# Kernel tuning notes

Measured on AMD Instinct MI355X. Metric: run time of the kernel, lower is better.

The kernel has to match this reference:

```python
import jax, jax.numpy as jnp
import numpy as np

F_IN, N_TREES, DEPTH, TREE_DIM, BATCH = 256, 512, 6, 3, 512


def entmax15_axis0(z):
    """Exact 1.5-entmax along axis 0 (sort-based algorithm from Peters et al. 2019)."""
    z = z / 2.0
    z = z - jnp.max(z, axis=0, keepdims=True)
    zs = -jnp.sort(-z, axis=0)                      # descending sort, [F, N]
    F = z.shape[0]
    rho = jnp.arange(1, F + 1, dtype=z.dtype)[:, None]
    mean = jnp.cumsum(zs, axis=0) / rho
    mean_sq = jnp.cumsum(zs * zs, axis=0) / rho
    ss = rho * (mean_sq - mean * mean)
    delta = (1.0 - ss) / rho
    tau = mean - jnp.sqrt(jnp.clip(delta, 0.0))
    support = (tau <= zs).astype(jnp.int32)
    k = jnp.sum(support, axis=0) - 1                # last valid index per column
    tau_star = jnp.take_along_axis(tau, k[None, :], axis=0)
    return jnp.square(jnp.clip(z - tau_star, 0.0))


def setup_inputs() -> dict:
    key = jax.random.key(0)
    k0, k1, k2, k3 = jax.random.split(key, 4)
    return {
        "input": jax.random.normal(k0, (BATCH, F_IN), jnp.float32),
        "feat_attention": jax.random.uniform(k1, (F_IN, N_TREES * DEPTH), jnp.float32),
        "feature_thresholds": jax.random.normal(k2, (N_TREES, DEPTH), jnp.float32) * 0.1,
        "log_temperatures": jnp.zeros((N_TREES, DEPTH), jnp.float32),
        "response": jax.random.normal(k3, (N_TREES, TREE_DIM, 2 ** DEPTH), jnp.float32),
    }


def reference(input, feat_attention, feature_thresholds, log_temperatures, response):
    T, D = feature_thresholds.shape
    F = feat_attention.shape[0]
    # sparse feature selection per (tree, depth)
    choice_weight = entmax15_axis0(feat_attention).reshape(F, T, D)
    feature_values = jnp.einsum('bi,ind->bnd', input, choice_weight)      # [B, T, D]
    # thresholding with learned temperature, bin_func == '05_01'
    tl = (feature_values - feature_thresholds) * jnp.exp(-log_temperatures)
    tl = jnp.stack([-tl, tl], axis=-1)                                    # [B, T, D, 2]
    bins = jnp.clip(0.5 * tl + 0.5, -0.5, 1.5)
    # binary codes of the 2^D leaves: [D, 2^D, 2]
    idx = jnp.arange(2 ** D)
    off = 2 ** jnp.arange(D)
    bc = ((idx[None, :] // off[:, None]) % 2).astype(bins.dtype)
    codes = jnp.stack([bc, 1.0 - bc], axis=-1)
    # depth-wise outer product into leaf weights
    bin_matches = jnp.einsum('btds,dcs->btdc', bins, codes)               # [B, T, D, 2^D]
    response_weights = jnp.prod(bin_matches, axis=-2)                     # [B, T, 2^D]
    out = jnp.einsum('bnd,ncd->bnc', response_weights, response)          # [B, T, C]
    return out.reshape(out.shape[0], -1)
```

## Files before the change

kernel.cpp:

```cpp
#include <hip/hip_runtime.h>
#include <math.h>

#define F_IN 256
#define NTREES 512
#define DEPTH 6
#define NCOLS (NTREES * DEPTH)
#define BATCH 512
#define OUTW (NTREES * 3)

typedef __attribute__((ext_vector_type(8))) short bf16x8;
typedef __attribute__((ext_vector_type(4))) float f32x4;
typedef __attribute__((ext_vector_type(8))) unsigned short u16x8;

__device__ __forceinline__ unsigned short f2bf(float x) {
    unsigned u = __float_as_uint(x);
    return (unsigned short)((u + 0x7FFFu + ((u >> 16) & 1u)) >> 16);
}
__device__ __forceinline__ void split2(float x, unsigned short& h, unsigned short& l) {
    h = f2bf(x);
    l = f2bf(x - __uint_as_float((unsigned)h << 16));
}

__global__ __launch_bounds__(256) void k_entmax(const float* __restrict__ att,
                                                unsigned short* __restrict__ cwT_hi,
                                                unsigned short* __restrict__ cwT_lo) {
    const int tid = threadIdx.x;
    const int n0 = blockIdx.x * 16;
    const int lane = tid & 63;
    const int w = tid >> 6;
    const int g = lane >> 4;
    const int li = lane & 15;

    __shared__ __align__(16) float s_z[16][260];

    const int cld = tid & 15;
#pragma unroll
    for (int it = 0; it < 16; ++it) {
        int f = (tid >> 4) + it * 16;
        s_z[cld][f] = att[f * NCOLS + n0 + cld];
    }
    __syncthreads();

    const int c = w * 4 + g;
    float4 z[4];
#pragma unroll
    for (int j = 0; j < 4; ++j) {
        float4 v = *(const float4*)&s_z[c][li * 16 + 4 * j];
        z[j] = make_float4(v.x * 0.5f, v.y * 0.5f, v.z * 0.5f, v.w * 0.5f);
    }
    float m = fmaxf(fmaxf(fmaxf(z[0].x, z[0].y), fmaxf(z[0].z, z[0].w)),
                    fmaxf(fmaxf(z[1].x, z[1].y), fmaxf(z[1].z, z[1].w)));
    m = fmaxf(m, fmaxf(fmaxf(fmaxf(z[2].x, z[2].y), fmaxf(z[2].z, z[2].w)),
                       fmaxf(fmaxf(z[3].x, z[3].y), fmaxf(z[3].z, z[3].w))));
#pragma unroll
    for (int off = 8; off >= 1; off >>= 1) m = fmaxf(m, __shfl_xor(m, off));
#pragma unroll
    for (int j = 0; j < 4; ++j) {
        z[j].x -= m; z[j].y -= m; z[j].z -= m; z[j].w -= m;
    }

    float tau = -1.0f;
    for (int iter = 0; iter < 14; ++iter) {
        float s1p[4], s2p[4];
#pragma unroll
        for (int j = 0; j < 4; ++j) {
            float d0 = fmaxf(z[j].x - tau, 0.f);
            float d1 = fmaxf(z[j].y - tau, 0.f);
            float d2 = fmaxf(z[j].z - tau, 0.f);
            float d3 = fmaxf(z[j].w - tau, 0.f);
            s1p[j] = (d0 + d1) + (d2 + d3);
            s2p[j] = fmaf(d0, d0, fmaf(d1, d1, fmaf(d2, d2, d3 * d3)));
        }
        float s1 = (s1p[0] + s1p[1]) + (s1p[2] + s1p[3]);
        float s2 = (s2p[0] + s2p[1]) + (s2p[2] + s2p[3]);
#pragma unroll
        for (int off = 8; off >= 1; off >>= 1) {
            s1 += __shfl_xor(s1, off);
            s2 += __shfl_xor(s2, off);
        }
        tau += (s2 - 1.f) / (2.f * s1);
        if (__all(fabsf(s2 - 1.f) < 4e-6f)) break;
    }

#pragma unroll
    for (int j = 0; j < 4; ++j) {
        float4 pv;
        float v0 = fmaxf(z[j].x - tau, 0.f);
        float v1 = fmaxf(z[j].y - tau, 0.f);
        float v2 = fmaxf(z[j].z - tau, 0.f);
        float v3 = fmaxf(z[j].w - tau, 0.f);
        pv.x = v0 * v0; pv.y = v1 * v1; pv.z = v2 * v2; pv.w = v3 * v3;
        *(float4*)&s_z[c][li * 16 + 4 * j] = pv;
    }
    __syncthreads();

    const int nl = tid >> 4;
    const int f0 = (tid & 15) * 16;
#pragma unroll
    for (int jj = 0; jj < 2; ++jj) {
        u16x8 hv, lv;
#pragma unroll
        for (int e = 0; e < 8; ++e) {
            unsigned short h, l;
            split2(s_z[nl][f0 + jj * 8 + e], h, l);
            hv[e] = h; lv[e] = l;
        }
        *(u16x8*)&cwT_hi[(n0 + nl) * F_IN + f0 + jj * 8] = hv;
        *(u16x8*)&cwT_lo[(n0 + nl) * F_IN + f0 + jj * 8] = lv;
    }
}

__global__ __launch_bounds__(512) void k_fused(const unsigned short* __restrict__ Ah,
                                               const unsigned short* __restrict__ Al,
                                               const float* __restrict__ inp,
                                               const float* __restrict__ thr,
                                               const float* __restrict__ ltemp,
                                               const float* __restrict__ resp,
                                               float* __restrict__ out) {
    const int tb  = blockIdx.x;
    const int b0  = blockIdx.y * 128;
    const int t0g = tb * 8;
    const int n0g = tb * 48;
    const int tid = threadIdx.x;
    const int wave = tid >> 6, lane = tid & 63;
    const int quad = lane >> 4, lr = lane & 15;

    __shared__ float sFV[48][132];
    __shared__ float sO[128][25];

    const int bw = b0 + wave * 16;
    const unsigned short* pah = Ah + (n0g + lr) * F_IN + quad * 8;
    const unsigned short* pal = Al + (n0g + lr) * F_IN + quad * 8;
    const float* pbf = inp + (bw + lr) * F_IN + quad * 8;

    f32x4 acc[3];
#pragma unroll
    for (int i = 0; i < 3; ++i) acc[i] = (f32x4){0.f, 0.f, 0.f, 0.f};

#pragma unroll
    for (int k0 = 0; k0 < F_IN; k0 += 32) {
        bf16x8 ah[3], al[3], bh, bl;
#pragma unroll
        for (int i = 0; i < 3; ++i) {
            ah[i] = *(const bf16x8*)(pah + i * 16 * F_IN + k0);
            al[i] = *(const bf16x8*)(pal + i * 16 * F_IN + k0);
        }
        float4 v0 = *(const float4*)(pbf + k0);
        float4 v1 = *(const float4*)(pbf + k0 + 4);
        float fb[8] = {v0.x, v0.y, v0.z, v0.w, v1.x, v1.y, v1.z, v1.w};
#pragma unroll
        for (int e = 0; e < 8; ++e) {
            unsigned short hh, ll;
            split2(fb[e], hh, ll);
            bh[e] = (short)hh; bl[e] = (short)ll;
        }
#pragma unroll
        for (int i = 0; i < 3; ++i) {
            acc[i] = __builtin_amdgcn_mfma_f32_16x16x32_bf16(ah[i], bh, acc[i], 0, 0, 0);
            acc[i] = __builtin_amdgcn_mfma_f32_16x16x32_bf16(ah[i], bl, acc[i], 0, 0, 0);
            acc[i] = __builtin_amdgcn_mfma_f32_16x16x32_bf16(al[i], bh, acc[i], 0, 0, 0);
        }
    }
#pragma unroll
    for (int i = 0; i < 3; ++i)
#pragma unroll
        for (int r = 0; r < 4; ++r)
            sFV[16 * i + quad * 4 + r][wave * 16 + lr] = acc[i][r];
    __syncthreads();

#pragma unroll
    for (int p = 0; p < 2; ++p) {
        const int pi = p * 512 + tid;
        const int tl = pi >> 7;
        const int b  = pi & 127;
        const int tls = __builtin_amdgcn_readfirstlane(tl);
        const float* rp = resp + (size_t)(t0g + tls) * 192;
        const float* tp = thr   + (t0g + tls) * 6;
        const float* lp = ltemp + (t0g + tls) * 6;

        float bpos[6], bneg[6];
#pragma unroll
        for (int d = 0; d < 6; ++d) {
            float fvv = sFV[tls * 6 + d][b];
            float tlv = (fvv - tp[d]) * __expf(-lp[d]);
            float hp = 0.5f * tlv + 0.5f;
            float hn = 0.5f - 0.5f * tlv;
            bpos[d] = fminf(fmaxf(hp, -0.5f), 1.5f);
            bneg[d] = fminf(fmaxf(hn, -0.5f), 1.5f);
        }
        float pr[64];
        pr[0] = 1.f;
#pragma unroll
        for (int d = 0; d < 6; ++d) {
            int half = 1 << d;
#pragma unroll 32
            for (int i = half - 1; i >= 0; --i) {
                float v = pr[i];
                pr[i + half] = v * bneg[d];
                pr[i]        = v * bpos[d];
            }
        }
        float a0 = 0.f, a1 = 0.f, a2 = 0.f;
#pragma unroll
        for (int cc = 0; cc < 64; ++cc) {
            a0 = fmaf(pr[cc], rp[cc], a0);
            a1 = fmaf(pr[cc], rp[64 + cc], a1);
            a2 = fmaf(pr[cc], rp[128 + cc], a2);
        }
        sO[b][tl * 3 + 0] = a0;
        sO[b][tl * 3 + 1] = a1;
        sO[b][tl * 3 + 2] = a2;
    }
    __syncthreads();
    for (int i = tid; i < 128 * 24; i += 512) {
        int row = i / 24, col = i % 24;
        out[(b0 + row) * OUTW + t0g * 3 + col] = sO[row][col];
    }
}

extern "C" void kernel_launch(void* const* d_in, const int* in_sizes, int n_in,
                              void* d_out, int out_size, void* d_ws, size_t ws_size,
                              hipStream_t stream) {
    const float* input = (const float*)d_in[0];
    const float* att   = (const float*)d_in[1];
    const float* thr   = (const float*)d_in[2];
    const float* ltemp = (const float*)d_in[3];
    const float* resp  = (const float*)d_in[4];
    float* out = (float*)d_out;

    unsigned short* cwT_hi = (unsigned short*)d_ws;
    unsigned short* cwT_lo = cwT_hi + NCOLS * F_IN;

    hipLaunchKernelGGL(k_entmax, dim3(NCOLS / 16), dim3(256), 0, stream,
                       att, cwT_hi, cwT_lo);
    hipLaunchKernelGGL(k_fused, dim3(NTREES / 8, BATCH / 128), dim3(512), 0, stream,
                       cwT_hi, cwT_lo, input, thr, ltemp, resp, out);
}
```

Baseline: 90.79 us.

## Fuse entmax into main kernel, computing weights in shared memory per block

Removes the separate entmax kernel and its global bf16 hi/lo workspace. Each block of the fused kernel now loads its 48 attention columns, runs the entmax bisection/Newton iteration in shared memory (8 threads per column), and splits to bf16 hi/lo on the fly when feeding MFMA. Shared memory is reused through a union for the later stages. This saves a launch and a global round trip, but entmax is recomputed redundantly by the 4 batch-tile blocks per tree group. Shared memory use per block also grows, which may lower occupancy.

```diff
diff --git a/kernel.cpp b/kernel.cpp
--- a/kernel.cpp
+++ b/kernel.cpp
@@ -10,7 +10,6 @@
 
 typedef __attribute__((ext_vector_type(8))) short bf16x8;
 typedef __attribute__((ext_vector_type(4))) float f32x4;
-typedef __attribute__((ext_vector_type(8))) unsigned short u16x8;
 
 __device__ __forceinline__ unsigned short f2bf(float x) {
     unsigned u = __float_as_uint(x);
@@ -21,102 +20,12 @@
     l = f2bf(x - __uint_as_float((unsigned)h << 16));
 }
 
-__global__ __launch_bounds__(256) void k_entmax(const float* __restrict__ att,
-                                                unsigned short* __restrict__ cwT_hi,
-                                                unsigned short* __restrict__ cwT_lo) {
-    const int tid = threadIdx.x;
-    const int n0 = blockIdx.x * 16;
-    const int lane = tid & 63;
-    const int w = tid >> 6;
-    const int g = lane >> 4;
-    const int li = lane & 15;
-
-    __shared__ __align__(16) float s_z[16][260];
-
-    const int cld = tid & 15;
-#pragma unroll
-    for (int it = 0; it < 16; ++it) {
-        int f = (tid >> 4) + it * 16;
-        s_z[cld][f] = att[f * NCOLS + n0 + cld];
-    }
-    __syncthreads();
-
-    const int c = w * 4 + g;
-    float4 z[4];
-#pragma unroll
-    for (int j = 0; j < 4; ++j) {
-        float4 v = *(const float4*)&s_z[c][li * 16 + 4 * j];
-        z[j] = make_float4(v.x * 0.5f, v.y * 0.5f, v.z * 0.5f, v.w * 0.5f);
-    }
-    float m = fmaxf(fmaxf(fmaxf(z[0].x, z[0].y), fmaxf(z[0].z, z[0].w)),
-                    fmaxf(fmaxf(z[1].x, z[1].y), fmaxf(z[1].z, z[1].w)));
-    m = fmaxf(m, fmaxf(fmaxf(fmaxf(z[2].x, z[2].y), fmaxf(z[2].z, z[2].w)),
-                       fmaxf(fmaxf(z[3].x, z[3].y), fmaxf(z[3].z, z[3].w))));
-#pragma unroll
-    for (int off = 8; off >= 1; off >>= 1) m = fmaxf(m, __shfl_xor(m, off));
-#pragma unroll
-    for (int j = 0; j < 4; ++j) {
-        z[j].x -= m; z[j].y -= m; z[j].z -= m; z[j].w -= m;
-    }
-
-    float tau = -1.0f;
-    for (int iter = 0; iter < 14; ++iter) {
-        float s1p[4], s2p[4];
-#pragma unroll
-        for (int j = 0; j < 4; ++j) {
-            float d0 = fmaxf(z[j].x - tau, 0.f);
-            float d1 = fmaxf(z[j].y - tau, 0.f);
-            float d2 = fmaxf(z[j].z - tau, 0.f);
-            float d3 = fmaxf(z[j].w - tau, 0.f);
-            s1p[j] = (d0 + d1) + (d2 + d3);
-            s2p[j] = fmaf(d0, d0, fmaf(d1, d1, fmaf(d2, d2, d3 * d3)));
-        }
-        float s1 = (s1p[0] + s1p[1]) + (s1p[2] + s1p[3]);
-        float s2 = (s2p[0] + s2p[1]) + (s2p[2] + s2p[3]);
-#pragma unroll
-        for (int off = 8; off >= 1; off >>= 1) {
-            s1 += __shfl_xor(s1, off);
-            s2 += __shfl_xor(s2, off);
-        }
-        tau += (s2 - 1.f) / (2.f * s1);
-        if (__all(fabsf(s2 - 1.f) < 4e-6f)) break;
-    }
-
-#pragma unroll
-    for (int j = 0; j < 4; ++j) {
-        float4 pv;
-        float v0 = fmaxf(z[j].x - tau, 0.f);
-        float v1 = fmaxf(z[j].y - tau, 0.f);
-        float v2 = fmaxf(z[j].z - tau, 0.f);
-        float v3 = fmaxf(z[j].w - tau, 0.f);
-        pv.x = v0 * v0; pv.y = v1 * v1; pv.z = v2 * v2; pv.w = v3 * v3;
-        *(float4*)&s_z[c][li * 16 + 4 * j] = pv;
-    }
-    __syncthreads();
-
-    const int nl = tid >> 4;
-    const int f0 = (tid & 15) * 16;
-#pragma unroll
-    for (int jj = 0; jj < 2; ++jj) {
-        u16x8 hv, lv;
-#pragma unroll
-        for (int e = 0; e < 8; ++e) {
-            unsigned short h, l;
-            split2(s_z[nl][f0 + jj * 8 + e], h, l);
-            hv[e] = h; lv[e] = l;
-        }
-        *(u16x8*)&cwT_hi[(n0 + nl) * F_IN + f0 + jj * 8] = hv;
-        *(u16x8*)&cwT_lo[(n0 + nl) * F_IN + f0 + jj * 8] = lv;
-    }
-}
-
-__global__ __launch_bounds__(512) void k_fused(const unsigned short* __restrict__ Ah,
-                                               const unsigned short* __restrict__ Al,
-                                               const float* __restrict__ inp,
-                                               const float* __restrict__ thr,
-                                               const float* __restrict__ ltemp,
-                                               const float* __restrict__ resp,
-                                               float* __restrict__ out) {
+__global__ __launch_bounds__(512) void k_all(const float* __restrict__ att,
+                                             const float* __restrict__ inp,
+                                             const float* __restrict__ thr,
+                                             const float* __restrict__ ltemp,
+                                             const float* __restrict__ resp,
+                                             float* __restrict__ out) {
     const int tb  = blockIdx.x;
     const int b0  = blockIdx.y * 128;
     const int t0g = tb * 8;
@@ -125,12 +34,82 @@
     const int wave = tid >> 6, lane = tid & 63;
     const int quad = lane >> 4, lr = lane & 15;
 
-    __shared__ float sFV[48][132];
-    __shared__ float sO[128][25];
+    __shared__ union {
+        float z[48][260];
+        struct { float fv[48][132]; float o[128][25]; } p2;
+    } s;
+
+    {
+        const int c4 = tid & 15;
+        const int fr = tid >> 4;
+        if (c4 < 12) {
+#pragma unroll
+            for (int it = 0; it < 8; ++it) {
+                int f = fr + it * 32;
+                float4 v = *(const float4*)&att[f * NCOLS + n0g + 4 * c4];
+                s.z[4 * c4 + 0][f] = v.x;
+                s.z[4 * c4 + 1][f] = v.y;
+                s.z[4 * c4 + 2][f] = v.z;
+                s.z[4 * c4 + 3][f] = v.w;
+            }
+        }
+    }
+    __syncthreads();
+
+    if (wave < 6) {
+        const int c  = tid >> 3;
+        const int li = tid & 7;
+        float4 z[8];
+#pragma unroll
+        for (int j = 0; j < 8; ++j) {
+            float4 v = *(const float4*)&s.z[c][li * 32 + 4 * j];
+            z[j] = make_float4(v.x * 0.5f, v.y * 0.5f, v.z * 0.5f, v.w * 0.5f);
+        }
+        float m = -1e30f;
+#pragma unroll
+        for (int j = 0; j < 8; ++j)
+            m = fmaxf(m, fmaxf(fmaxf(z[j].x, z[j].y), fmaxf(z[j].z, z[j].w)));
+#pragma unroll
+        for (int off = 4; off >= 1; off >>= 1) m = fmaxf(m, __shfl_xor(m, off));
+#pragma unroll
+        for (int j = 0; j < 8; ++j) {
+            z[j].x -= m; z[j].y -= m; z[j].z -= m; z[j].w -= m;
+        }
+
+        float tau = -1.0f;
+        for (int iter = 0; iter < 14; ++iter) {
+            float s1 = 0.f, s2 = 0.f;
+#pragma unroll
+            for (int j = 0; j < 8; ++j) {
+                float d0 = fmaxf(z[j].x - tau, 0.f);
+                float d1 = fmaxf(z[j].y - tau, 0.f);
+                float d2 = fmaxf(z[j].z - tau, 0.f);
+                float d3 = fmaxf(z[j].w - tau, 0.f);
+                s1 += (d0 + d1) + (d2 + d3);
+                s2 = fmaf(d0, d0, fmaf(d1, d1, fmaf(d2, d2, fmaf(d3, d3, s2))));
+            }
+#pragma unroll
+            for (int off = 4; off >= 1; off >>= 1) {
+                s1 += __shfl_xor(s1, off);
+                s2 += __shfl_xor(s2, off);
+            }
+            tau += (s2 - 1.f) / (2.f * s1);
+            if (__all(fabsf(s2 - 1.f) < 4e-6f)) break;
+        }
+#pragma unroll
+        for (int j = 0; j < 8; ++j) {
+            float v0 = fmaxf(z[j].x - tau, 0.f);
+            float v1 = fmaxf(z[j].y - tau, 0.f);
+            float v2 = fmaxf(z[j].z - tau, 0.f);
+            float v3 = fmaxf(z[j].w - tau, 0.f);
+            float4 pv;
+            pv.x = v0 * v0; pv.y = v1 * v1; pv.z = v2 * v2; pv.w = v3 * v3;
+            *(float4*)&s.z[c][li * 32 + 4 * j] = pv;
+        }
+    }
+    __syncthreads();
 
     const int bw = b0 + wave * 16;
-    const unsigned short* pah = Ah + (n0g + lr) * F_IN + quad * 8;
-    const unsigned short* pal = Al + (n0g + lr) * F_IN + quad * 8;
     const float* pbf = inp + (bw + lr) * F_IN + quad * 8;
 
     f32x4 acc[3];
@@ -142,8 +121,15 @@
         bf16x8 ah[3], al[3], bh, bl;
 #pragma unroll
         for (int i = 0; i < 3; ++i) {
-            ah[i] = *(const bf16x8*)(pah + i * 16 * F_IN + k0);
-            al[i] = *(const bf16x8*)(pal + i * 16 * F_IN + k0);
+            float4 a0 = *(const float4*)&s.z[16 * i + lr][quad * 8 + k0];
+            float4 a1 = *(const float4*)&s.z[16 * i + lr][quad * 8 + k0 + 4];
+            float fa[8] = {a0.x, a0.y, a0.z, a0.w, a1.x, a1.y, a1.z, a1.w};
+#pragma unroll
+            for (int e = 0; e < 8; ++e) {
+                unsigned short hh, ll;
+                split2(fa[e], hh, ll);
+                ah[i][e] = (short)hh; al[i][e] = (short)ll;
+            }
         }
         float4 v0 = *(const float4*)(pbf + k0);
         float4 v1 = *(const float4*)(pbf + k0 + 4);
@@ -161,11 +147,13 @@
             acc[i] = __builtin_amdgcn_mfma_f32_16x16x32_bf16(al[i], bh, acc[i], 0, 0, 0);
         }
     }
+    __syncthreads();
+
 #pragma unroll
     for (int i = 0; i < 3; ++i)
 #pragma unroll
         for (int r = 0; r < 4; ++r)
-            sFV[16 * i + quad * 4 + r][wave * 16 + lr] = acc[i][r];
+            s.p2.fv[16 * i + quad * 4 + r][wave * 16 + lr] = acc[i][r];
     __syncthreads();
 
 #pragma unroll
@@ -174,14 +162,14 @@
         const int tl = pi >> 7;
         const int b  = pi & 127;
         const int tls = __builtin_amdgcn_readfirstlane(tl);
-        const float* rp = resp + (size_t)(t0g + tls) * 192;
+        const float* rp = resp  + (size_t)(t0g + tls) * 192;
         const float* tp = thr   + (t0g + tls) * 6;
         const float* lp = ltemp + (t0g + tls) * 6;
 
         float bpos[6], bneg[6];
 #pragma unroll
         for (int d = 0; d < 6; ++d) {
-            float fvv = sFV[tls * 6 + d][b];
+            float fvv = s.p2.fv[tls * 6 + d][b];
             float tlv = (fvv - tp[d]) * __expf(-lp[d]);
             float hp = 0.5f * tlv + 0.5f;
             float hn = 0.5f - 0.5f * tlv;
@@ -207,14 +195,14 @@
             a1 = fmaf(pr[cc], rp[64 + cc], a1);
             a2 = fmaf(pr[cc], rp[128 + cc], a2);
         }
-        sO[b][tl * 3 + 0] = a0;
-        sO[b][tl * 3 + 1] = a1;
-        sO[b][tl * 3 + 2] = a2;
+        s.p2.o[b][tl * 3 + 0] = a0;
+        s.p2.o[b][tl * 3 + 1] = a1;
+        s.p2.o[b][tl * 3 + 2] = a2;
     }
     __syncthreads();
     for (int i = tid; i < 128 * 24; i += 512) {
         int row = i / 24, col = i % 24;
-        out[(b0 + row) * OUTW + t0g * 3 + col] = sO[row][col];
+        out[(b0 + row) * OUTW + t0g * 3 + col] = s.p2.o[row][col];
     }
 }
 
@@ -227,12 +215,8 @@
     const float* ltemp = (const float*)d_in[3];
     const float* resp  = (const float*)d_in[4];
     float* out = (float*)d_out;
-
-    unsigned short* cwT_hi = (unsigned short*)d_ws;
-    unsigned short* cwT_lo = cwT_hi + NCOLS * F_IN;
-
-    hipLaunchKernelGGL(k_entmax, dim3(NCOLS / 16), dim3(256), 0, stream,
-                       att, cwT_hi, cwT_lo);
-    hipLaunchKernelGGL(k_fused, dim3(NTREES / 8, BATCH / 128), dim3(512), 0, stream,
-                       cwT_hi, cwT_lo, input, thr, ltemp, resp, out);
-}
+    (void)d_ws; (void)ws_size;
+
+    hipLaunchKernelGGL(k_all, dim3(NTREES / 8, BATCH / 128), dim3(512), 0, stream,
+                       att, input, thr, ltemp, resp, out);
+}
```

Result: faster. 86.41 us (-4.8%).
